# Optimization experiments

Measured on AMD Instinct MI355X. Metric: run time of the kernel, lower is better.

The kernel has to match this reference:

```python
import jax, jax.numpy as jnp
import numpy as np

A, B, I, J, K = 8, 256, 256, 256, 256  # a=batch, b=tokens, i=s-channels, j=c-channels, k=out_dim


def setup_inputs() -> dict:
    key = jax.random.key(0)
    k1, k2, k3 = jax.random.split(key, 3)
    input_s = jax.random.normal(k1, (A, B, I), dtype=jnp.float32)
    input_c = jax.random.normal(k2, (B, J), dtype=jnp.float32)
    # learned params: w ~ N(0, 0.02), b zeros (as in build())
    w = jax.random.normal(k3, (I, J, K), dtype=jnp.float32) * 0.02
    b = jnp.zeros((K,), dtype=jnp.float32)
    return {"input_s": input_s, "input_c": input_c, "w": w, "b": b}


def reference(input_s, input_c, w, b):
    # Original: tmp = einsum('abi,ijk->abjk', input_s, w); out = einsum('bj,abjk->abk', input_c, tmp) + b
    # Mathematically identical fused bilinear contraction (avoids the [a,b,j,k] intermediate):
    out = jnp.einsum('abi,bj,ijk->abk', input_s, input_c, w)
    return out + b
```

## Files before the change

### kernel.cpp

```cpp
#include <hip/hip_runtime.h>
#include <hip/hip_bf16.h>

#define A_ 8
#define B_ 256
#define I_ 256
#define J_ 256
#define K_ 256

typedef __attribute__((ext_vector_type(8))) short short8_t;
typedef __attribute__((ext_vector_type(4))) float f32x4_t;

static __device__ __forceinline__ uint pack2bf(float a, float b) {
  float2 f2; f2.x = a; f2.y = b;
  __hip_bfloat162 h2 = __float22bfloat162_rn(f2);
  uint r;
  __builtin_memcpy(&r, &h2, 4);
  return r;
}

static __device__ __forceinline__ ushort f2bf(float f) {
  __hip_bfloat16 h = __float2bfloat16(f);
  ushort us;
  __builtin_memcpy(&us, &h, 2);
  return us;
}

static __device__ __forceinline__ float bf2f(ushort h) {
  uint u = ((uint)h) << 16;
  float f;
  __builtin_memcpy(&f, &u, 4);
  return f;
}

__global__ __launch_bounds__(256) void prepass_c_kernel(
    const float* __restrict__ c, ushort* __restrict__ cbf) {
  const int idx = blockIdx.x * 256 + threadIdx.x;
  const f32x4_t v = *reinterpret_cast<const f32x4_t*>(c + (size_t)idx * 4);
  uint2 r;
  r.x = pack2bf(v[0], v[1]);
  r.y = pack2bf(v[2], v[3]);
  *reinterpret_cast<uint2*>(cbf + (size_t)idx * 4) = r;
}

__global__ __launch_bounds__(256, 2) void pass1_kernel(
    const ushort* __restrict__ cbf, const float* __restrict__ w,
    ushort* __restrict__ u) {
  const int i    = blockIdx.x;
  const int kh   = blockIdx.y;
  const int tid  = threadIdx.x;
  const int lane = tid & 63;
  const int wave = tid >> 6;
  const int lrow = lane & 15;
  const int lhi  = lane >> 4;

  __shared__ __align__(16) char Bt[128 * 512];

  const float* wi = w + (size_t)i * (J_ * K_) + kh * 128;

  const int jp = tid & 63;
  const int kc = tid >> 6;
  const int arow = wave * 64 + lrow;

  f32x4_t acc[4][8];
#pragma unroll
  for (int m = 0; m < 4; m++)
#pragma unroll
    for (int n = 0; n < 8; n++) acc[m][n] = (f32x4_t)(0.0f);

  f32x4_t sv[8];

#define GLOAD(jh, ko)                                                       \
  {                                                                         \
    _Pragma("unroll") for (int jj = 0; jj < 2; jj++)                        \
        _Pragma("unroll") for (int q = 0; q < 4; q++)                       \
        sv[jj * 4 + q] = *reinterpret_cast<const f32x4_t*>(                 \
            wi + (size_t)((jh) * 128 + jp * 2 + jj) * K_ + kc * 32 + (ko) + \
            q * 4);                                                         \
  }
#define STORE(jh, ko)                                                       \
  {                                                                         \
    const int jc  = (jh) * 64 + jp;                                         \
    const int cid = jc >> 2;                                                \
    const int wb  = (jc & 3) * 4;                                           \
    _Pragma("unroll") for (int q = 0; q < 16; q++) {                        \
      const int k = kc * 32 + (ko) + q;                                     \
      *reinterpret_cast<uint*>(                                             \
          Bt + k * 512 + ((cid ^ (q & 7)) * 16) + wb) =                     \
          pack2bf(sv[(q >> 2)][q & 3], sv[4 + (q >> 2)][q & 3]);            \
    }                                                                       \
  }
#define COMPUTE(jh, kk)                                                     \
  {                                                                         \
    short8_t af[4];                                                         \
    _Pragma("unroll") for (int m = 0; m < 4; m++)                           \
        af[m] = *reinterpret_cast<const short8_t*>(                         \
            cbf + (size_t)(arow + m * 16) * J_ + (jh) * 128 + (kk) * 32 +   \
            lhi * 8);                                                       \
    short8_t bf[8];                                                         \
    _Pragma("unroll") for (int n = 0; n < 8; n++) {                         \
      const int row = n * 16 + lrow;                                        \
      const int cid = ((jh) * 16 + (kk) * 4 + lhi) ^ (lrow & 7);            \
      bf[n] = *reinterpret_cast<const short8_t*>(Bt + row * 512 + cid * 16);\
    }                                                                       \
    _Pragma("unroll") for (int m = 0; m < 4; m++)                           \
        _Pragma("unroll") for (int n = 0; n < 8; n++)                       \
        acc[m][n] = __builtin_amdgcn_mfma_f32_16x16x32_bf16(                \
            af[m], bf[n], acc[m][n], 0, 0, 0);                              \
  }

  GLOAD(0, 0);  STORE(0, 0);
  GLOAD(0, 16); STORE(0, 16);
  __syncthreads();

  GLOAD(1, 0);
  COMPUTE(0, 0);
  COMPUTE(0, 1);
  STORE(1, 0);
  GLOAD(1, 16);
  COMPUTE(0, 2);
  COMPUTE(0, 3);
  STORE(1, 16);
  __syncthreads();

  COMPUTE(1, 0);
  COMPUTE(1, 1);
  COMPUTE(1, 2);
  COMPUTE(1, 3);

#undef GLOAD
#undef STORE
#undef COMPUTE

#pragma unroll
  for (int m = 0; m < 4; m++) {
    const int brow = wave * 64 + m * 16 + lhi * 4;
#pragma unroll
    for (int n = 0; n < 8; n++) {
      const int kc_g = kh * 128 + n * 16 + lrow;
      ushort* up = u + ((size_t)brow * I_ + i) * K_ + kc_g;
#pragma unroll
      for (int r = 0; r < 4; r++)
        up[(size_t)r * (I_ * K_)] = f2bf(acc[m][n][r]);
    }
  }
}

__global__ __launch_bounds__(256) void pass2_kernel(
    const float* __restrict__ s, const ushort* __restrict__ u,
    const float* __restrict__ bias, float* __restrict__ out) {
  const int b   = blockIdx.x;
  const int a0  = blockIdx.y * 4;
  const int tid = threadIdx.x;
  __shared__ float s_l[4][I_];
  __shared__ float red[8][4][K_];

#pragma unroll
  for (int v = 0; v < 4; v++) {
    const int idx = tid + v * 256;
    const int a = idx >> 8, ii = idx & 255;
    s_l[a][ii] = s[((size_t)(a0 + a) * B_ + b) * I_ + ii];
  }
  __syncthreads();

  const int kb = (tid & 31) * 8;
  const int ig = tid >> 5;
  float acc[4][8];
#pragma unroll
  for (int a = 0; a < 4; a++)
#pragma unroll
    for (int q = 0; q < 8; q++) acc[a][q] = 0.0f;

  const ushort* ub = u + ((size_t)b * I_ + ig * 32) * K_ + kb;
  for (int ii = 0; ii < 32; ++ii) {
    const short8_t uv = *reinterpret_cast<const short8_t*>(ub + (size_t)ii * K_);
    float f[8];
#pragma unroll
    for (int q = 0; q < 8; q++) f[q] = bf2f((ushort)uv[q]);
    const int i = ig * 32 + ii;
#pragma unroll
    for (int a = 0; a < 4; a++) {
      const float sa = s_l[a][i];
#pragma unroll
      for (int q = 0; q < 8; q++) acc[a][q] += sa * f[q];
    }
  }

#pragma unroll
  for (int a = 0; a < 4; a++) {
    f32x4_t r0, r1;
#pragma unroll
    for (int q = 0; q < 4; q++) { r0[q] = acc[a][q]; r1[q] = acc[a][4 + q]; }
    *reinterpret_cast<f32x4_t*>(&red[ig][a][kb])     = r0;
    *reinterpret_cast<f32x4_t*>(&red[ig][a][kb + 4]) = r1;
  }
  __syncthreads();

#pragma unroll
  for (int v = 0; v < 4; v++) {
    const int k = tid;
    float sum = 0.0f;
#pragma unroll
    for (int g = 0; g < 8; g++) sum += red[g][v][k];
    out[((size_t)(a0 + v) * B_ + b) * K_ + k] = sum + bias[k];
  }
}

__global__ __launch_bounds__(256) void fallback_kernel(
    const float* __restrict__ s, const float* __restrict__ cmat,
    const float* __restrict__ w, const float* __restrict__ bias,
    float* __restrict__ out) {
  const int b = blockIdx.x;
  const int k = threadIdx.x;
  __shared__ float c_l[J_];
  __shared__ float s_l[A_][I_];
  for (int idx = threadIdx.x; idx < J_; idx += 256) c_l[idx] = cmat[(size_t)b * J_ + idx];
  for (int idx = threadIdx.x; idx < A_ * I_; idx += 256) {
    const int a = idx >> 8;
    const int i = idx & 255;
    s_l[a][i] = s[(size_t)a * (B_ * I_) + (size_t)b * I_ + i];
  }
  __syncthreads();
  float acc[A_];
#pragma unroll
  for (int a = 0; a < A_; a++) acc[a] = 0.0f;
  for (int i = 0; i < I_; i++) {
    const float* wrow = w + (size_t)i * (J_ * K_) + k;
    float inner = 0.0f;
    for (int j = 0; j < J_; j++) inner += c_l[j] * wrow[(size_t)j * K_];
#pragma unroll
    for (int a = 0; a < A_; a++) acc[a] += s_l[a][i] * inner;
  }
#pragma unroll
  for (int a = 0; a < A_; a++)
    out[((size_t)a * B_ + b) * K_ + k] = acc[a] + bias[k];
}

extern "C" void kernel_launch(void* const* d_in, const int* in_sizes, int n_in,
                              void* d_out, int out_size, void* d_ws, size_t ws_size,
                              hipStream_t stream) {
  const float* s    = (const float*)d_in[0];
  const float* cmat = (const float*)d_in[1];
  const float* w    = (const float*)d_in[2];
  const float* bias = (const float*)d_in[3];
  float* out = (float*)d_out;

  const size_t u_elems   = (size_t)B_ * I_ * K_;
  const size_t cbf_elems = (size_t)B_ * J_;
  const size_t need = (u_elems + cbf_elems) * sizeof(ushort);

  if (ws_size >= need) {
    ushort* u   = (ushort*)d_ws;
    ushort* cbf = (ushort*)d_ws + u_elems;
    prepass_c_kernel<<<dim3((B_ * J_) / (256 * 4)), dim3(256), 0, stream>>>(cmat, cbf);
    pass1_kernel<<<dim3(I_, 2), dim3(256), 0, stream>>>(cbf, w, u);
    pass2_kernel<<<dim3(B_, 2), dim3(256), 0, stream>>>(s, u, bias, out);
  } else {
    fallback_kernel<<<dim3(B_), dim3(256), 0, stream>>>(s, cmat, w, bias, out);
  }
}
```

Measured before the change: 46.81 us.

## Merge k-halves into one 512-thread block with row-major padded LDS weight tile

Pass1 now processes the whole 256-wide k range per i in a single 512-thread block (8 waves split over b and k) instead of two 256-thread blocks. The weight slice is staged as row-major bf16 in a padded 256x258 LDS array with fully coalesced global reads, replacing the transposed swizzled layout. The aim is simpler, coalesced staging and one block per i. The cost is that B fragments are now assembled from eight scalar 16-bit LDS reads each rather than one vector read, the grid halves to 256 blocks, and the LDS footprint grows to about 129 KB.

```diff
diff --git a/kernel.cpp b/kernel.cpp
--- a/kernel.cpp
+++ b/kernel.cpp
@@ -42,24 +42,22 @@
   *reinterpret_cast<uint2*>(cbf + (size_t)idx * 4) = r;
 }
 
-__global__ __launch_bounds__(256, 2) void pass1_kernel(
+__global__ __launch_bounds__(512, 1) void pass1_kernel(
     const ushort* __restrict__ cbf, const float* __restrict__ w,
     ushort* __restrict__ u) {
   const int i    = blockIdx.x;
-  const int kh   = blockIdx.y;
   const int tid  = threadIdx.x;
   const int lane = tid & 63;
-  const int wave = tid >> 6;
+  const int wv   = tid >> 6;
+  const int wb   = wv & 3;
+  const int wk   = wv >> 2;
   const int lrow = lane & 15;
   const int lhi  = lane >> 4;
 
-  __shared__ __align__(16) char Bt[128 * 512];
-
-  const float* wi = w + (size_t)i * (J_ * K_) + kh * 128;
-
-  const int jp = tid & 63;
-  const int kc = tid >> 6;
-  const int arow = wave * 64 + lrow;
+  __shared__ ushort Wl[256][258];
+
+  const float* wi = w + (size_t)i * (J_ * K_);
+  const int arow = wb * 64 + lrow;
 
   f32x4_t acc[4][8];
 #pragma unroll
@@ -67,40 +65,34 @@
 #pragma unroll
     for (int n = 0; n < 8; n++) acc[m][n] = (f32x4_t)(0.0f);
 
-  f32x4_t sv[8];
-
-#define GLOAD(jh, ko)                                                       \
+  f32x4_t sA[8], sB[8];
+
+#define STAGE(r0, sq, CNT)                                                  \
   {                                                                         \
-    _Pragma("unroll") for (int jj = 0; jj < 2; jj++)                        \
-        _Pragma("unroll") for (int q = 0; q < 4; q++)                       \
-        sv[jj * 4 + q] = *reinterpret_cast<const f32x4_t*>(                 \
-            wi + (size_t)((jh) * 128 + jp * 2 + jj) * K_ + kc * 32 + (ko) + \
-            q * 4);                                                         \
-  }
-#define STORE(jh, ko)                                                       \
+    _Pragma("unroll") for (int q = 0; q < (CNT); q++)                       \
+        sq[q] = *reinterpret_cast<const f32x4_t*>(                          \
+            wi + (size_t)((r0) + q) * K_ + 4 * lane);                       \
+  }
+#define WRITE(r0, sq, CNT)                                                  \
   {                                                                         \
-    const int jc  = (jh) * 64 + jp;                                         \
-    const int cid = jc >> 2;                                                \
-    const int wb  = (jc & 3) * 4;                                           \
-    _Pragma("unroll") for (int q = 0; q < 16; q++) {                        \
-      const int k = kc * 32 + (ko) + q;                                     \
-      *reinterpret_cast<uint*>(                                             \
-          Bt + k * 512 + ((cid ^ (q & 7)) * 16) + wb) =                     \
-          pack2bf(sv[(q >> 2)][q & 3], sv[4 + (q >> 2)][q & 3]);            \
+    _Pragma("unroll") for (int q = 0; q < (CNT); q++) {                     \
+      uint2 val;                                                            \
+      val.x = pack2bf(sq[q][0], sq[q][1]);                                  \
+      val.y = pack2bf(sq[q][2], sq[q][3]);                                  \
+      *reinterpret_cast<uint2*>(&Wl[(r0) + q][4 * lane]) = val;             \
     }                                                                       \
   }
-#define COMPUTE(jh, kk)                                                     \
+#define STEP(t)                                                             \
   {                                                                         \
     short8_t af[4];                                                         \
     _Pragma("unroll") for (int m = 0; m < 4; m++)                           \
         af[m] = *reinterpret_cast<const short8_t*>(                         \
-            cbf + (size_t)(arow + m * 16) * J_ + (jh) * 128 + (kk) * 32 +   \
-            lhi * 8);                                                       \
+            cbf + (size_t)(arow + m * 16) * J_ + (t) * 32 + lhi * 8);       \
     short8_t bf[8];                                                         \
     _Pragma("unroll") for (int n = 0; n < 8; n++) {                         \
-      const int row = n * 16 + lrow;                                        \
-      const int cid = ((jh) * 16 + (kk) * 4 + lhi) ^ (lrow & 7);            \
-      bf[n] = *reinterpret_cast<const short8_t*>(Bt + row * 512 + cid * 16);\
+      const int col = wk * 128 + n * 16 + lrow;                             \
+      _Pragma("unroll") for (int e = 0; e < 8; e++)                         \
+          bf[n][e] = (short)Wl[(t) * 32 + lhi * 8 + e][col];                \
     }                                                                       \
     _Pragma("unroll") for (int m = 0; m < 4; m++)                           \
         _Pragma("unroll") for (int n = 0; n < 8; n++)                       \
@@ -108,36 +100,44 @@
             af[m], bf[n], acc[m][n], 0, 0, 0);                              \
   }
 
-  GLOAD(0, 0);  STORE(0, 0);
-  GLOAD(0, 16); STORE(0, 16);
-  __syncthreads();
-
-  GLOAD(1, 0);
-  COMPUTE(0, 0);
-  COMPUTE(0, 1);
-  STORE(1, 0);
-  GLOAD(1, 16);
-  COMPUTE(0, 2);
-  COMPUTE(0, 3);
-  STORE(1, 16);
-  __syncthreads();
-
-  COMPUTE(1, 0);
-  COMPUTE(1, 1);
-  COMPUTE(1, 2);
-  COMPUTE(1, 3);
-
-#undef GLOAD
-#undef STORE
-#undef COMPUTE
+  const int h0 = wv * 16;
+  STAGE(h0, sA, 8);
+  STAGE(h0 + 8, sB, 8);
+  WRITE(h0, sA, 8);
+  WRITE(h0 + 8, sB, 8);
+  __syncthreads();
+
+  const int h1 = 128 + wv * 16;
+  STAGE(h1, sA, 4);
+  STEP(0);
+  WRITE(h1, sA, 4);
+  STAGE(h1 + 4, sB, 4);
+  STEP(1);
+  WRITE(h1 + 4, sB, 4);
+  STAGE(h1 + 8, sA, 4);
+  STEP(2);
+  WRITE(h1 + 8, sA, 4);
+  STAGE(h1 + 12, sB, 4);
+  STEP(3);
+  WRITE(h1 + 12, sB, 4);
+  __syncthreads();
+
+  STEP(4);
+  STEP(5);
+  STEP(6);
+  STEP(7);
+
+#undef STAGE
+#undef WRITE
+#undef STEP
 
 #pragma unroll
   for (int m = 0; m < 4; m++) {
-    const int brow = wave * 64 + m * 16 + lhi * 4;
+    const int brow = wb * 64 + m * 16 + lhi * 4;
 #pragma unroll
     for (int n = 0; n < 8; n++) {
-      const int kc_g = kh * 128 + n * 16 + lrow;
-      ushort* up = u + ((size_t)brow * I_ + i) * K_ + kc_g;
+      const int kc = wk * 128 + n * 16 + lrow;
+      ushort* up = u + ((size_t)brow * I_ + i) * K_ + kc;
 #pragma unroll
       for (int r = 0; r < 4; r++)
         up[(size_t)r * (I_ * K_)] = f2bf(acc[m][n][r]);
@@ -252,7 +252,7 @@
     ushort* u   = (ushort*)d_ws;
     ushort* cbf = (ushort*)d_ws + u_elems;
     prepass_c_kernel<<<dim3((B_ * J_) / (256 * 4)), dim3(256), 0, stream>>>(cmat, cbf);
-    pass1_kernel<<<dim3(I_, 2), dim3(256), 0, stream>>>(cbf, w, u);
+    pass1_kernel<<<dim3(I_), dim3(512), 0, stream>>>(cbf, w, u);
     pass2_kernel<<<dim3(B_, 2), dim3(256), 0, stream>>>(s, u, bias, out);
   } else {
     fallback_kernel<<<dim3(B_), dim3(256), 0, stream>>>(s, cmat, w, bias, out);
```

Measured after the change: 43.86 us. 6.3% less time.
